# Performance work log

Measured on AMD Instinct MI355X. Metric: run time of the kernel, lower is better.

The kernel has to match this reference:

```python
import jax, jax.numpy as jnp
import numpy as np

EPS_LOG = 1e-08   # module's eps added inside the log
EPS_PD = 1e-06    # torch.nn.PairwiseDistance default eps (added to the difference)


def setup_inputs() -> dict:
    key = jax.random.key(0)
    x = jax.random.normal(key, (16384, 512), dtype=jnp.float32)
    return {"x": x}


def reference(x):
    n = x.shape[0]
    # Pairwise dot products; mask diagonal with -1 (as in the torch code)
    dots = jnp.matmul(x, x.T)  # [n, n]
    dots = jnp.where(jnp.eye(n, dtype=bool), jnp.float32(-1.0), dots)
    I = jnp.argmax(dots, axis=1)  # nearest neighbor index per row (no grad)
    # torch PairwiseDistance(2): ||x1 - x2 + eps||_2 with eps=1e-6
    diff = x - x[I] + EPS_PD  # [n, d]
    rho = jnp.sqrt(jnp.sum(diff * diff, axis=1))  # [n]
    loss = -jnp.mean(jnp.log(rho + EPS_LOG))
    return loss
```

## Files before the change

kernel.cpp:

```cpp
#include <hip/hip_runtime.h>
#include <stdint.h>

#define N_ROWS 16384
#define DIM    512

typedef int v4i __attribute__((ext_vector_type(4)));
typedef unsigned long long u64;
typedef unsigned char u8;

__device__ __forceinline__ void gload_lds16(const void* g, void* l) {
    __builtin_amdgcn_global_load_lds(
        (const __attribute__((address_space(1))) unsigned int*)g,
        (__attribute__((address_space(3))) unsigned int*)l,
        16, 0, 0);
}

__global__ __launch_bounds__(256)
void convert_i8_kernel(const float* __restrict__ x, unsigned* __restrict__ x8,
                       u64* __restrict__ table, float* __restrict__ out) {
    int tid    = blockIdx.x * blockDim.x + threadIdx.x;
    int stride = gridDim.x * blockDim.x;
    if (tid < N_ROWS) table[tid] = 0;
    if (tid == 0) out[0] = 0.f;
    const float4* x4 = (const float4*)x;
    const int n4 = (N_ROWS * DIM) / 4;
    for (int i = tid; i < n4; i += stride) {
        float4 v = x4[i];
        int a = (int)rintf(fminf(fmaxf(v.x * 31.75f, -127.f), 127.f));
        int b = (int)rintf(fminf(fmaxf(v.y * 31.75f, -127.f), 127.f));
        int c = (int)rintf(fminf(fmaxf(v.z * 31.75f, -127.f), 127.f));
        int d = (int)rintf(fminf(fmaxf(v.w * 31.75f, -127.f), 127.f));
        x8[i] = (unsigned)((a & 0xFF) | ((b & 0xFF) << 8) | ((c & 0xFF) << 16) | (d << 24));
    }
}

__global__ __launch_bounds__(256)
void argmax_dots_kernel(const u8* __restrict__ xb, u64* __restrict__ table) {
    __shared__ __attribute__((aligned(16))) u8 ldsA[128 * 128];
    __shared__ __attribute__((aligned(16))) u8 ldsB[128 * 128];

    const int u = blockIdx.x >> 6;
    const int p = blockIdx.x & 63;
    const int rT = (u <= p) ? (127 - p) : p;
    const int cT = (u <= p) ? (127 - u) : (u - 1);

    const int t      = threadIdx.x;
    const int lane   = t & 63;
    const int wave   = t >> 6;
    const int lane15 = lane & 15;
    const int quad   = lane >> 4;
    const int rh = wave >> 1;
    const int ch = wave & 1;

    const int rowBase = rT * 128;
    const int colBase = cT * 128;

    const u8* gA[4];
    const u8* gB[4];
#pragma unroll
    for (int j = 0; j < 4; ++j) {
        const int G   = j * 256 + t;
        const int row = ((G >> 9) << 6) + (((G >> 6) & 3) << 4) + (G & 15);
        const int kc  = (((G >> 8) & 1) << 2) + ((G >> 4) & 3);
        gA[j] = xb + (size_t)(rowBase + row) * DIM + kc * 16;
        gB[j] = xb + (size_t)(colBase + row) * DIM + kc * 16;
    }
    const int dstOff = wave * 1024;

    v4i acc[4][4];
#pragma unroll
    for (int rf = 0; rf < 4; ++rf)
#pragma unroll
        for (int cf = 0; cf < 4; ++cf) {
            v4i z = {0, 0, 0, 0};
            acc[rf][cf] = z;
        }

#pragma unroll
    for (int k = 0; k < 4; ++k) {
        const int kk = k * 128;
#pragma unroll
        for (int j = 0; j < 4; ++j) {
            gload_lds16(gA[j] + kk, (char*)ldsA + j * 4096 + dstOff);
            gload_lds16(gB[j] + kk, (char*)ldsB + j * 4096 + dstOff);
        }
        __syncthreads();

#pragma unroll
        for (int s = 0; s < 2; ++s) {
            v4i a8[4], b8[4];
#pragma unroll
            for (int rf = 0; rf < 4; ++rf)
                a8[rf] = *(const v4i*)(ldsA + rh * 8192 + s * 4096 + rf * 1024 + lane * 16);
#pragma unroll
            for (int cf = 0; cf < 4; ++cf)
                b8[cf] = *(const v4i*)(ldsB + ch * 8192 + s * 4096 + cf * 1024 + lane * 16);
#pragma unroll
            for (int rf = 0; rf < 4; ++rf)
#pragma unroll
                for (int cf = 0; cf < 4; ++cf)
                    acc[rf][cf] = __builtin_amdgcn_mfma_i32_16x16x64_i8(
                        a8[rf], b8[cf], acc[rf][cf], 0, 0, 0);
        }
        __syncthreads();
    }

    const int colLane = colBase + ch * 64 + lane15;
#pragma unroll
    for (int rf = 0; rf < 4; ++rf) {
#pragma unroll
        for (int e = 0; e < 4; ++e) {
            const int row = rowBase + rh * 64 + rf * 16 + quad * 4 + e;
            int bv = -2147483647;
            int bc = 0;
#pragma unroll
            for (int cf = 0; cf < 4; ++cf) {
                const int v = acc[rf][cf][e];
                const int col = colLane + cf * 16;
                if (v > bv && col != row) { bv = v; bc = col; }
            }
            u64 packed = ((u64)((unsigned)bv ^ 0x80000000u) << 32) | (unsigned)(~bc);
#pragma unroll
            for (int m = 1; m < 16; m <<= 1) {
                u64 o = __shfl_xor(packed, m, 64);
                if (o > packed) packed = o;
            }
            if (lane15 == 0) atomicMax(&table[row], packed);
        }
    }

    if (rT != cT) {
#pragma unroll
        for (int cf = 0; cf < 4; ++cf) {
            const int col = colLane + cf * 16;
            int bv = -2147483647;
            int br_ = 0;
#pragma unroll
            for (int rf = 0; rf < 4; ++rf)
#pragma unroll
                for (int e = 0; e < 4; ++e) {
                    const int v = acc[rf][cf][e];
                    const int row = rowBase + rh * 64 + rf * 16 + quad * 4 + e;
                    if (v > bv) { bv = v; br_ = row; }
                }
            u64 packed = ((u64)((unsigned)bv ^ 0x80000000u) << 32) | (unsigned)(~br_);
            u64 o = __shfl_xor(packed, 16, 64); if (o > packed) packed = o;
            o     = __shfl_xor(packed, 32, 64); if (o > packed) packed = o;
            if (quad == 0) atomicMax(&table[col], packed);
        }
    }
}

__global__ __launch_bounds__(256)
void rho_loss_kernel(const float* __restrict__ x, const u64* __restrict__ table,
                     float* __restrict__ out) {
    const int lane = threadIdx.x & 63;
    const int wave = threadIdx.x >> 6;
    const int waveGlobal = blockIdx.x * 4 + wave;

    float local = 0.f;
    for (int r8 = 0; r8 < 8; ++r8) {
        const int row = waveGlobal * 8 + r8;
        const u64 packed = table[row];
        const int nb = (int)(~(unsigned)(packed & 0xFFFFFFFFu));

        const float4* xr = (const float4*)(x + (size_t)row * DIM);
        const float4* xn = (const float4*)(x + (size_t)nb  * DIM);
        float s = 0.f;
#pragma unroll
        for (int tt = 0; tt < 2; ++tt) {
            float4 a = xr[lane * 2 + tt];
            float4 b = xn[lane * 2 + tt];
            float d0 = a.x - b.x + 1e-6f;
            float d1 = a.y - b.y + 1e-6f;
            float d2 = a.z - b.z + 1e-6f;
            float d3 = a.w - b.w + 1e-6f;
            s += d0 * d0 + d1 * d1 + d2 * d2 + d3 * d3;
        }
#pragma unroll
        for (int m = 1; m < 64; m <<= 1) s += __shfl_xor(s, m, 64);

        if (lane == 0) {
            float rho = sqrtf(s);
            local += logf(rho + 1e-8f);
        }
    }
    if (lane == 0) atomicAdd(out, -local * (1.0f / 16384.0f));
}

extern "C" void kernel_launch(void* const* d_in, const int* in_sizes, int n_in,
                              void* d_out, int out_size, void* d_ws, size_t ws_size,
                              hipStream_t stream) {
    const float* x = (const float*)d_in[0];

    u8*    xb    = (u8*)d_ws;
    u64*   table = (u64*)((char*)d_ws + (size_t)N_ROWS * DIM);
    float* out   = (float*)d_out;

    convert_i8_kernel<<<2048, 256, 0, stream>>>(x, (unsigned*)xb, table, out);
    argmax_dots_kernel<<<8256, 256, 0, stream>>>(xb, table);
    rho_loss_kernel<<<512, 256, 0, stream>>>(x, table, out);
}
```

Before: 266.4 us.

## Give each wave private LDS tiles and prefetch the next K-chunk without block barriers

The int8 dot-product argmax kernel drops block-shared 128x128 LDS tiles. Each wave now loads its own 64 A rows and 64 B rows in 64-byte K chunks into a private LDS region. The next chunk's global-to-LDS loads are issued after the current chunk is read into registers, so they overlap the MFMAs, and all __syncthreads are removed in favour of per-wave waitcnt. The trade-off is that A and B halves are no longer shared between waves, which doubles global/L2 load traffic. There are also more, shorter K steps, and each one waits for its loads to finish.

```diff
diff --git a/kernel.cpp b/kernel.cpp
--- a/kernel.cpp
+++ b/kernel.cpp
@@ -36,36 +36,33 @@
 
 __global__ __launch_bounds__(256)
 void argmax_dots_kernel(const u8* __restrict__ xb, u64* __restrict__ table) {
-    __shared__ __attribute__((aligned(16))) u8 ldsA[128 * 128];
-    __shared__ __attribute__((aligned(16))) u8 ldsB[128 * 128];
+    __shared__ __attribute__((aligned(16))) u8 lds[4 * 8192];
 
     const int u = blockIdx.x >> 6;
     const int p = blockIdx.x & 63;
     const int rT = (u <= p) ? (127 - p) : p;
     const int cT = (u <= p) ? (127 - u) : (u - 1);
 
-    const int t      = threadIdx.x;
-    const int lane   = t & 63;
-    const int wave   = t >> 6;
+    const int lane   = threadIdx.x & 63;
+    const int wave   = threadIdx.x >> 6;
     const int lane15 = lane & 15;
     const int quad   = lane >> 4;
     const int rh = wave >> 1;
     const int ch = wave & 1;
 
-    const int rowBase = rT * 128;
-    const int colBase = cT * 128;
+    const int rowBase = rT * 128 + rh * 64;
+    const int colBase = cT * 128 + ch * 64;
+
+    u8* ldsA = lds + wave * 8192;
+    u8* ldsB = ldsA + 4096;
 
     const u8* gA[4];
     const u8* gB[4];
 #pragma unroll
-    for (int j = 0; j < 4; ++j) {
-        const int G   = j * 256 + t;
-        const int row = ((G >> 9) << 6) + (((G >> 6) & 3) << 4) + (G & 15);
-        const int kc  = (((G >> 8) & 1) << 2) + ((G >> 4) & 3);
-        gA[j] = xb + (size_t)(rowBase + row) * DIM + kc * 16;
-        gB[j] = xb + (size_t)(colBase + row) * DIM + kc * 16;
-    }
-    const int dstOff = wave * 1024;
+    for (int rf = 0; rf < 4; ++rf) {
+        gA[rf] = xb + (size_t)(rowBase + rf * 16 + lane15) * DIM + quad * 16;
+        gB[rf] = xb + (size_t)(colBase + rf * 16 + lane15) * DIM + quad * 16;
+    }
 
     v4i acc[4][4];
 #pragma unroll
@@ -77,40 +74,48 @@
         }
 
 #pragma unroll
-    for (int k = 0; k < 4; ++k) {
-        const int kk = k * 128;
-#pragma unroll
-        for (int j = 0; j < 4; ++j) {
-            gload_lds16(gA[j] + kk, (char*)ldsA + j * 4096 + dstOff);
-            gload_lds16(gB[j] + kk, (char*)ldsB + j * 4096 + dstOff);
-        }
-        __syncthreads();
-
-#pragma unroll
-        for (int s = 0; s < 2; ++s) {
-            v4i a8[4], b8[4];
-#pragma unroll
-            for (int rf = 0; rf < 4; ++rf)
-                a8[rf] = *(const v4i*)(ldsA + rh * 8192 + s * 4096 + rf * 1024 + lane * 16);
+    for (int rf = 0; rf < 4; ++rf) {
+        gload_lds16(gA[rf], ldsA + rf * 1024);
+        gload_lds16(gB[rf], ldsB + rf * 1024);
+    }
+
+#pragma unroll
+    for (int k = 0; k < 8; ++k) {
+        asm volatile("s_waitcnt vmcnt(0)" ::: "memory");
+
+        v4i a8[4], b8[4];
+#pragma unroll
+        for (int rf = 0; rf < 4; ++rf)
+            a8[rf] = *(const v4i*)(ldsA + rf * 1024 + lane * 16);
+#pragma unroll
+        for (int cf = 0; cf < 4; ++cf)
+            b8[cf] = *(const v4i*)(ldsB + cf * 1024 + lane * 16);
+
+        asm volatile("s_waitcnt lgkmcnt(0)" ::: "memory");
+
+        if (k < 7) {
+            const int kk = (k + 1) * 64;
+#pragma unroll
+            for (int rf = 0; rf < 4; ++rf) {
+                gload_lds16(gA[rf] + kk, ldsA + rf * 1024);
+                gload_lds16(gB[rf] + kk, ldsB + rf * 1024);
+            }
+        }
+
+#pragma unroll
+        for (int rf = 0; rf < 4; ++rf)
 #pragma unroll
             for (int cf = 0; cf < 4; ++cf)
-                b8[cf] = *(const v4i*)(ldsB + ch * 8192 + s * 4096 + cf * 1024 + lane * 16);
-#pragma unroll
-            for (int rf = 0; rf < 4; ++rf)
-#pragma unroll
-                for (int cf = 0; cf < 4; ++cf)
-                    acc[rf][cf] = __builtin_amdgcn_mfma_i32_16x16x64_i8(
-                        a8[rf], b8[cf], acc[rf][cf], 0, 0, 0);
-        }
-        __syncthreads();
-    }
-
-    const int colLane = colBase + ch * 64 + lane15;
+                acc[rf][cf] = __builtin_amdgcn_mfma_i32_16x16x64_i8(
+                    a8[rf], b8[cf], acc[rf][cf], 0, 0, 0);
+    }
+
+    const int colLane = colBase + lane15;
 #pragma unroll
     for (int rf = 0; rf < 4; ++rf) {
 #pragma unroll
         for (int e = 0; e < 4; ++e) {
-            const int row = rowBase + rh * 64 + rf * 16 + quad * 4 + e;
+            const int row = rowBase + rf * 16 + quad * 4 + e;
             int bv = -2147483647;
             int bc = 0;
 #pragma unroll
@@ -140,7 +145,7 @@
 #pragma unroll
                 for (int e = 0; e < 4; ++e) {
                     const int v = acc[rf][cf][e];
-                    const int row = rowBase + rh * 64 + rf * 16 + quad * 4 + e;
+                    const int row = rowBase + rf * 16 + quad * 4 + e;
                     if (v > bv) { bv = v; br_ = row; }
                 }
             u64 packed = ((u64)((unsigned)bv ^ 0x80000000u) << 32) | (unsigned)(~br_);
```

New measurement: 384.5 us. 1.44x slower.

## Replace global atomicMax argmax merging with per-tile partials and a reduce kernel

Applied to the files above, without the earlier changes.

Each tile of the int8 Gram matrix first reduces its row-wise and column-wise best (value, index) packs in LDS across the two column or row halves. It then writes them to a 128×N partial buffer with plain stores instead of doing contended 64-bit atomicMax on the shared table. A new reduce kernel takes the max over the 128 partials per row, which also removes the table zeroing from the convert kernel. This trades atomic contention for about 16 MB of extra global writes and reads, an extra kernel launch, and a small, low-parallelism reduction grid.

```diff
diff --git a/kernel.cpp b/kernel.cpp
--- a/kernel.cpp
+++ b/kernel.cpp
@@ -17,10 +17,9 @@
 
 __global__ __launch_bounds__(256)
 void convert_i8_kernel(const float* __restrict__ x, unsigned* __restrict__ x8,
-                       u64* __restrict__ table, float* __restrict__ out) {
+                       float* __restrict__ out) {
     int tid    = blockIdx.x * blockDim.x + threadIdx.x;
     int stride = gridDim.x * blockDim.x;
-    if (tid < N_ROWS) table[tid] = 0;
     if (tid == 0) out[0] = 0.f;
     const float4* x4 = (const float4*)x;
     const int n4 = (N_ROWS * DIM) / 4;
@@ -35,7 +34,7 @@
 }
 
 __global__ __launch_bounds__(256)
-void argmax_dots_kernel(const u8* __restrict__ xb, u64* __restrict__ table) {
+void argmax_dots_kernel(const u8* __restrict__ xb, u64* __restrict__ part) {
     __shared__ __attribute__((aligned(16))) u8 ldsA[128 * 128];
     __shared__ __attribute__((aligned(16))) u8 ldsB[128 * 128];
 
@@ -125,11 +124,19 @@
                 u64 o = __shfl_xor(packed, m, 64);
                 if (o > packed) packed = o;
             }
-            if (lane15 == 0) atomicMax(&table[row], packed);
-        }
+            if (lane15 == 0)
+                ((u64*)ldsA)[(ch * 128) + rh * 64 + rf * 16 + quad * 4 + e] = packed;
+        }
+    }
+    __syncthreads();
+    if (t < 128) {
+        u64 v0 = ((u64*)ldsA)[t];
+        u64 v1 = ((u64*)ldsA)[128 + t];
+        part[(size_t)cT * N_ROWS + rowBase + t] = (v0 > v1) ? v0 : v1;
     }
 
     if (rT != cT) {
+        __syncthreads();
 #pragma unroll
         for (int cf = 0; cf < 4; ++cf) {
             const int col = colLane + cf * 16;
@@ -146,9 +153,28 @@
             u64 packed = ((u64)((unsigned)bv ^ 0x80000000u) << 32) | (unsigned)(~br_);
             u64 o = __shfl_xor(packed, 16, 64); if (o > packed) packed = o;
             o     = __shfl_xor(packed, 32, 64); if (o > packed) packed = o;
-            if (quad == 0) atomicMax(&table[col], packed);
-        }
-    }
+            if (quad == 0)
+                ((u64*)ldsB)[(rh * 128) + ch * 64 + cf * 16 + lane15] = packed;
+        }
+        __syncthreads();
+        if (t < 128) {
+            u64 v0 = ((u64*)ldsB)[t];
+            u64 v1 = ((u64*)ldsB)[128 + t];
+            part[(size_t)rT * N_ROWS + colBase + t] = (v0 > v1) ? v0 : v1;
+        }
+    }
+}
+
+__global__ __launch_bounds__(256)
+void reduce_part_kernel(const u64* __restrict__ part, u64* __restrict__ table) {
+    const int r = blockIdx.x * blockDim.x + threadIdx.x;
+    u64 best = part[r];
+#pragma unroll 8
+    for (int s = 1; s < 128; ++s) {
+        u64 v = part[(size_t)s * N_ROWS + r];
+        if (v > best) best = v;
+    }
+    table[r] = best;
 }
 
 __global__ __launch_bounds__(256)
@@ -194,10 +220,12 @@
     const float* x = (const float*)d_in[0];
 
     u8*    xb    = (u8*)d_ws;
-    u64*   table = (u64*)((char*)d_ws + (size_t)N_ROWS * DIM);
+    u64*   part  = (u64*)((char*)d_ws + (size_t)N_ROWS * DIM);
+    u64*   table = part + (size_t)128 * N_ROWS;
     float* out   = (float*)d_out;
 
-    convert_i8_kernel<<<2048, 256, 0, stream>>>(x, (unsigned*)xb, table, out);
-    argmax_dots_kernel<<<8256, 256, 0, stream>>>(xb, table);
+    convert_i8_kernel<<<2048, 256, 0, stream>>>(x, (unsigned*)xb, out);
+    argmax_dots_kernel<<<8256, 256, 0, stream>>>(xb, part);
+    reduce_part_kernel<<<64, 256, 0, stream>>>(part, table);
     rho_loss_kernel<<<512, 256, 0, stream>>>(x, table, out);
 }
```

After: 272.1 us. 2.1% more time.
